# Kernel optimization log

Measured on AMD Instinct MI355X. Metric: run time of the kernel, lower is better.

## Reference

```python
import jax, jax.numpy as jnp
import numpy as np

N_HEADS = 32
N_KV_HEADS = 8
HEAD_DIM = 128
HIDDEN = 4096
ROPE_BASE = 10000.0


def _rope_tables(seq_len, head_dim, base):
    inv_freq = 1.0 / (base ** (jnp.arange(0, head_dim, 2, dtype=jnp.float32) / head_dim))
    t = jnp.arange(seq_len, dtype=jnp.float32)
    freqs = jnp.outer(t, inv_freq)                    # (S, D/2)
    emb = jnp.concatenate([freqs, freqs], axis=-1)    # (S, D)
    return jnp.cos(emb), jnp.sin(emb)


def _rotate_half(x):
    half = x.shape[-1] // 2
    return jnp.concatenate([-x[..., half:], x[..., :half]], axis=-1)


def _apply_rope(x, cos, sin):
    # x: (B, H, S, D); cos/sin: (S, D)
    return x * cos[None, None] + _rotate_half(x) * sin[None, None]


def setup_inputs() -> dict:
    key = jax.random.key(0)
    k1, k2, k3 = jax.random.split(key, 3)
    bsz, q_len = 2, 2048
    total_heads = N_HEADS + 2 * N_KV_HEADS
    hidden_states = jax.random.normal(k1, (bsz, q_len, HIDDEN), dtype=jnp.float32)
    w_qkv = jax.random.normal(k2, (total_heads * HEAD_DIM, HIDDEN), dtype=jnp.float32) * 0.02
    w_o = jax.random.normal(k3, (HIDDEN, N_HEADS * HEAD_DIM), dtype=jnp.float32) * 0.02
    return {"hidden_states": hidden_states, "w_qkv": w_qkv, "w_o": w_o}


def reference(hidden_states, w_qkv, w_o):
    bsz, q_len, _ = hidden_states.shape
    n_rep = N_HEADS // N_KV_HEADS

    qkv = jnp.einsum('bsh,oh->bso', hidden_states, w_qkv)  # (B, S, total_heads*D)
    q_sz = N_HEADS * HEAD_DIM
    kv_sz = N_KV_HEADS * HEAD_DIM
    q = qkv[..., :q_sz].reshape(bsz, q_len, N_HEADS, HEAD_DIM).transpose(0, 2, 1, 3)
    k = qkv[..., q_sz:q_sz + kv_sz].reshape(bsz, q_len, N_KV_HEADS, HEAD_DIM).transpose(0, 2, 1, 3)
    v = qkv[..., q_sz + kv_sz:].reshape(bsz, q_len, N_KV_HEADS, HEAD_DIM).transpose(0, 2, 1, 3)

    cos, sin = _rope_tables(q_len, HEAD_DIM, ROPE_BASE)
    q = _apply_rope(q, cos, sin)
    k = _apply_rope(k, cos, sin)

    # repeat KV heads for GQA
    k = jnp.repeat(k, n_rep, axis=1)  # (B, H, S, D)
    v = jnp.repeat(v, n_rep, axis=1)

    scale = HEAD_DIM ** -0.5
    scores = jnp.einsum('bhqd,bhkd->bhqk', q, k) * scale
    causal = jnp.tril(jnp.ones((q_len, q_len), dtype=bool))
    scores = jnp.where(causal[None, None], scores, jnp.finfo(scores.dtype).min)
    attn = jax.nn.softmax(scores, axis=-1)
    out = jnp.einsum('bhqk,bhkd->bhqd', attn, v)  # (B, H, S, D)
    out = out.transpose(0, 2, 1, 3).reshape(bsz, q_len, N_HEADS * HEAD_DIM)
    return jnp.einsum('bso,ho->bsh', out, w_o)
```

## Files before the change

kernel.cpp:

```cpp
#include <hip/hip_runtime.h>
#include <stdint.h>

#define N_HEADS   32
#define N_KV      8
#define HEAD_DIM  128
#define HIDDEN_DIM 4096
#define BSZ       2
#define SEQ       2048
#define TOT_HEADS 48
#define QKV_DIM   6144
#define ROWS      4096
#define ROPE_HEADS 40

typedef __attribute__((ext_vector_type(4)))  float f32x4;
typedef __attribute__((ext_vector_type(16))) float f32x16;
typedef __attribute__((ext_vector_type(8)))  short bf16x8;
typedef unsigned short u16;
typedef unsigned int   u32;

#define AS1 __attribute__((address_space(1)))
#define AS3 __attribute__((address_space(3)))

static __device__ __forceinline__ float bf16f(u16 u) { return __uint_as_float(((u32)u) << 16); }
static __device__ __forceinline__ u16 f2bf(float f) {
  u32 x = __float_as_uint(f);
  x += 0x7fffu + ((x >> 16) & 1u);
  return (u16)(x >> 16);
}
static __device__ __forceinline__ u32 cvt_pk_bf16(float lo, float hi) {
  u32 r;
  asm("v_cvt_pk_bf16_f32 %0, %1, %2" : "=v"(r) : "v"(lo), "v"(hi));
  return r;
}
static __device__ __forceinline__ bf16x8 mk8(u32 a, u32 b, u32 c, u32 d) {
  union { u32 u[4]; bf16x8 v; } x;
  x.u[0] = a; x.u[1] = b; x.u[2] = c; x.u[3] = d;
  return x.v;
}
static __device__ __forceinline__ void pl32swap(u32& a, u32& b) {
  asm("v_permlane32_swap_b32 %0, %1" : "+v"(a), "+v"(b));
}
static __device__ __forceinline__ float crosshalf_max(float v) {
  u32 xa = __float_as_uint(v), xb;
  asm("v_mov_b32 %0, %1" : "=v"(xb) : "v"(xa));
  pl32swap(xa, xb);
  return fmaxf(__uint_as_float(xa), __uint_as_float(xb));
}
static __device__ __forceinline__ float crosshalf_sum(float v) {
  u32 xa = __float_as_uint(v), xb;
  asm("v_mov_b32 %0, %1" : "=v"(xb) : "v"(xa));
  pl32swap(xa, xb);
  return __uint_as_float(xa) + __uint_as_float(xb);
}

#define SBAR()  do { __builtin_amdgcn_sched_barrier(0); __builtin_amdgcn_s_barrier(); \
                     __builtin_amdgcn_sched_barrier(0); } while (0)
#define LGKM0() do { asm volatile("s_waitcnt lgkmcnt(0)" ::: "memory"); \
                     __builtin_amdgcn_sched_barrier(0); } while (0)

__global__ void cast3_k(const float4* __restrict__ a, const float4* __restrict__ b,
                        const float4* __restrict__ c,
                        ushort4* __restrict__ oa, ushort4* __restrict__ ob,
                        ushort4* __restrict__ oc, int na, int nb, int nc) {
  int i = blockIdx.x * blockDim.x + threadIdx.x;
  const int stride = gridDim.x * blockDim.x;
  const int tot = na + nb + nc;
  for (; i < tot; i += stride) {
    const float4* s; ushort4* d; int j = i;
    if (j < na)           { s = a; d = oa; }
    else if (j < na + nb) { s = b; d = ob; j -= na; }
    else                  { s = c; d = oc; j -= na + nb; }
    const float4 v = s[j];
    ushort4 o;
    o.x = f2bf(v.x); o.y = f2bf(v.y); o.z = f2bf(v.z); o.w = f2bf(v.w);
    d[j] = o;
  }
}

__global__ void rope_tables_k(float* __restrict__ ctab, float* __restrict__ stab) {
  int t = blockIdx.x * blockDim.x + threadIdx.x;
  if (t >= SEQ * 64) return;
  int s = t >> 6, i = t & 63;
  float inv = powf(10000.0f, -(float)i / 64.0f);
  float ang = (float)s * inv;
  float sv, cv;
  sincosf(ang, &sv, &cv);
  ctab[t] = cv; stab[t] = sv;
}

template<int F32OUT>
__global__ __launch_bounds__(256, 2)
void gemm_bt_k(const u16* __restrict__ A, const u16* __restrict__ Bw,
               void* __restrict__ C, int M, int N, int K, int ldc)
{
  __shared__ uint4 smA[1024];
  __shared__ uint4 smB[1024];
  const int tid = threadIdx.x;
  const int nbx = N >> 7;
  const int bm = (blockIdx.x / nbx) << 7;
  const int bn = (blockIdx.x % nbx) << 7;
  const int lane = tid & 63;
  const int wave = tid >> 6;
  const int wm = (wave >> 1) << 6;
  const int wn = (wave & 1) << 6;
  const int fr = lane & 15;
  const int fq = lane >> 4;

  f32x4 acc[4][4];
#pragma unroll
  for (int i = 0; i < 4; ++i)
#pragma unroll
    for (int j = 0; j < 4; ++j)
      acc[i][j] = {0.f, 0.f, 0.f, 0.f};

  const int gl_r = lane >> 3;
  const int gl_c = (lane & 7) ^ gl_r;

  for (int k0 = 0; k0 < K; k0 += 64) {
#pragma unroll
    for (int i = 0; i < 4; ++i) {
      const int rbase = (wave << 5) + (i << 3);
      const int row = rbase + gl_r;
      const u16* gA = A  + (size_t)(bm + row) * K + k0 + (gl_c << 3);
      const u16* gB = Bw + (size_t)(bn + row) * K + k0 + (gl_c << 3);
      __builtin_amdgcn_global_load_lds((const AS1 u32*)gA, (AS3 u32*)&smA[rbase << 3], 16, 0, 0);
      __builtin_amdgcn_global_load_lds((const AS1 u32*)gB, (AS3 u32*)&smB[rbase << 3], 16, 0, 0);
    }
    __syncthreads();
#pragma unroll
    for (int kk = 0; kk < 2; ++kk) {
      bf16x8 af[4], bfr[4];
      const int cc = (kk << 2) + fq;
#pragma unroll
      for (int m = 0; m < 4; ++m) {
        const int row = wm + (m << 4) + fr;
        af[m] = *reinterpret_cast<const bf16x8*>(&smA[(row << 3) + (cc ^ (row & 7))]);
      }
#pragma unroll
      for (int n = 0; n < 4; ++n) {
        const int row = wn + (n << 4) + fr;
        bfr[n] = *reinterpret_cast<const bf16x8*>(&smB[(row << 3) + (cc ^ (row & 7))]);
      }
#pragma unroll
      for (int m = 0; m < 4; ++m)
#pragma unroll
        for (int n = 0; n < 4; ++n)
          acc[m][n] = __builtin_amdgcn_mfma_f32_16x16x32_bf16(af[m], bfr[n], acc[m][n], 0, 0, 0);
    }
    __syncthreads();
  }

  const int col0 = bn + wn + fr;
#pragma unroll
  for (int m = 0; m < 4; ++m) {
#pragma unroll
    for (int i = 0; i < 4; ++i) {
      const int row = bm + wm + (m << 4) + (fq << 2) + i;
      if (F32OUT) {
        float* rp = reinterpret_cast<float*>(C) + (size_t)row * ldc + col0;
#pragma unroll
        for (int n = 0; n < 4; ++n) rp[n << 4] = acc[m][n][i];
      } else {
        u16* rp = reinterpret_cast<u16*>(C) + (size_t)row * ldc + col0;
#pragma unroll
        for (int n = 0; n < 4; ++n) rp[n << 4] = f2bf(acc[m][n][i]);
      }
    }
  }
}

template<int F32OUT>
__global__ __launch_bounds__(512, 2)
void gemm256_k(const u16* __restrict__ A, const u16* __restrict__ Bw,
               void* __restrict__ C, int M, int N, int K, int ldc)
{
  extern __shared__ uint4 lds[];
  uint4* LA = lds;
  uint4* LB = lds + 4096;
  const int NT = K >> 6;
  const int tid  = threadIdx.x;
  const int lane = tid & 63;
  const int wave = tid >> 6;
  const int nbx = N >> 8;
  const int cpx = gridDim.x >> 3;
  const int wg  = (blockIdx.x & 7) * cpx + (blockIdx.x >> 3);
  const int bm = (wg / nbx) << 8;
  const int bn = (wg % nbx) << 8;

  const int wm = (wave >> 2) << 7;
  const int wn = (wave & 3) << 6;
  const int fr = lane & 15;
  const int fq = lane >> 4;
  const int s7 = fr & 7;

  const int rA  = (wave << 3) + (lane >> 3);
  const int c8e = (((lane & 7) ^ (lane >> 3)) << 3);

  auto SA = [&](int t, int h, int buf) {
    uint4* d = LA + (buf << 11) + (h << 10) + (wave << 6);
    const u16* s = A + (size_t)(bm + (h << 7) + rA) * K + (t << 6) + c8e;
    __builtin_amdgcn_global_load_lds((const AS1 u32*)s, (AS3 u32*)d, 16, 0, 0);
    __builtin_amdgcn_global_load_lds((const AS1 u32*)(s + (size_t)64 * K), (AS3 u32*)(d + 512), 16, 0, 0);
  };
  auto SB = [&](int t, int h, int buf) {
    uint4* d = LB + (buf << 11) + (h << 10) + (wave << 6);
    const u16* s = Bw + (size_t)(bn + (h << 7) + rA) * K + (t << 6) + c8e;
    __builtin_amdgcn_global_load_lds((const AS1 u32*)s, (AS3 u32*)d, 16, 0, 0);
    __builtin_amdgcn_global_load_lds((const AS1 u32*)(s + (size_t)64 * K), (AS3 u32*)(d + 512), 16, 0, 0);
  };

  f32x4 acc[8][4];
#pragma unroll
  for (int m = 0; m < 8; ++m)
#pragma unroll
    for (int n = 0; n < 4; ++n)
      acc[m][n] = {0.f, 0.f, 0.f, 0.f};

  SB(0, 0, 0); SB(0, 1, 0); SA(0, 0, 0); SA(0, 1, 0);
  SB(1, 0, 1); SB(1, 1, 1); SA(1, 0, 1);
  asm volatile("s_waitcnt vmcnt(6)" ::: "memory");
  SBAR();

  bf16x8 Af[4][2], B0[2][2], B1[2][2];

#pragma unroll 1
  for (int t = 0; t < NT; ++t) {
    const int buf  = t & 1;
    const int base = buf << 11;
    const int abase = base + ((wm + fr) << 3);
    const int bbase = base + ((wn + fr) << 3);

#pragma unroll
    for (int m = 0; m < 4; ++m)
#pragma unroll
      for (int kk = 0; kk < 2; ++kk)
        Af[m][kk] = *reinterpret_cast<const bf16x8*>(&LA[abase + m * 128 + (((kk << 2) + fq) ^ s7)]);
#pragma unroll
    for (int n = 0; n < 2; ++n)
#pragma unroll
      for (int kk = 0; kk < 2; ++kk)
        B0[n][kk] = *reinterpret_cast<const bf16x8*>(&LB[bbase + n * 128 + (((kk << 2) + fq) ^ s7)]);
    if (t + 1 < NT) SA(t + 1, 1, buf ^ 1);
    SBAR();
    LGKM0();
    __builtin_amdgcn_s_setprio(1);
#pragma unroll
    for (int m = 0; m < 4; ++m)
#pragma unroll
      for (int n = 0; n < 2; ++n)
#pragma unroll
        for (int kk = 0; kk < 2; ++kk)
          acc[m][n] = __builtin_amdgcn_mfma_f32_16x16x32_bf16(Af[m][kk], B0[n][kk], acc[m][n], 0, 0, 0);
    __builtin_amdgcn_s_setprio(0);
    SBAR();

#pragma unroll
    for (int n = 0; n < 2; ++n)
#pragma unroll
      for (int kk = 0; kk < 2; ++kk)
        B1[n][kk] = *reinterpret_cast<const bf16x8*>(&LB[bbase + (2 + n) * 128 + (((kk << 2) + fq) ^ s7)]);
    SBAR();
    LGKM0();
    __builtin_amdgcn_s_setprio(1);
#pragma unroll
    for (int m = 0; m < 4; ++m)
#pragma unroll
      for (int n = 0; n < 2; ++n)
#pragma unroll
        for (int kk = 0; kk < 2; ++kk)
          acc[m][2 + n] = __builtin_amdgcn_mfma_f32_16x16x32_bf16(Af[m][kk], B1[n][kk], acc[m][2 + n], 0, 0, 0);
    __builtin_amdgcn_s_setprio(0);
    SBAR();

#pragma unroll
    for (int m = 0; m < 4; ++m)
#pragma unroll
      for (int kk = 0; kk < 2; ++kk)
        Af[m][kk] = *reinterpret_cast<const bf16x8*>(&LA[abase + 512 + m * 128 + (((kk << 2) + fq) ^ s7)]);
    if (t + 2 < NT) SB(t + 2, 0, buf);
    SBAR();
    LGKM0();
    __builtin_amdgcn_s_setprio(1);
#pragma unroll
    for (int m = 0; m < 4; ++m)
#pragma unroll
      for (int n = 0; n < 2; ++n)
#pragma unroll
        for (int kk = 0; kk < 2; ++kk)
          acc[4 + m][2 + n] = __builtin_amdgcn_mfma_f32_16x16x32_bf16(Af[m][kk], B1[n][kk], acc[4 + m][2 + n], 0, 0, 0);
    __builtin_amdgcn_s_setprio(0);
    SBAR();

    if (t + 2 < NT) { SB(t + 2, 1, buf); SA(t + 2, 0, buf); }
    __builtin_amdgcn_s_setprio(1);
#pragma unroll
    for (int m = 0; m < 4; ++m)
#pragma unroll
      for (int n = 0; n < 2; ++n)
#pragma unroll
        for (int kk = 0; kk < 2; ++kk)
          acc[4 + m][n] = __builtin_amdgcn_mfma_f32_16x16x32_bf16(Af[m][kk], B0[n][kk], acc[4 + m][n], 0, 0, 0);
    __builtin_amdgcn_s_setprio(0);
    if (t < NT - 2)       { asm volatile("s_waitcnt vmcnt(6)" ::: "memory"); }
    else if (t == NT - 2) { asm volatile("s_waitcnt vmcnt(0)" ::: "memory"); }
    SBAR();
  }

  const int col0 = bn + wn + fr;
#pragma unroll
  for (int m = 0; m < 8; ++m) {
#pragma unroll
    for (int i = 0; i < 4; ++i) {
      const int row = bm + wm + (m << 4) + (fq << 2) + i;
      if (F32OUT) {
        float* rp = reinterpret_cast<float*>(C) + (size_t)row * ldc + col0;
#pragma unroll
        for (int n = 0; n < 4; ++n) rp[n << 4] = acc[m][n][i];
      } else {
        u16* rp = reinterpret_cast<u16*>(C) + (size_t)row * ldc + col0;
#pragma unroll
        for (int n = 0; n < 4; ++n) rp[n << 4] = f2bf(acc[m][n][i]);
      }
    }
  }
}

__global__ void rope_scatter_k(const u16* __restrict__ QKV,
                               const float* __restrict__ ctab, const float* __restrict__ stab,
                               u16* __restrict__ Qo, u16* __restrict__ Ko)
{
  const int t = blockIdx.x * blockDim.x + threadIdx.x;
  const int d = t & 63;
  const int hh = (t >> 6) % ROPE_HEADS;
  const int row = t / (64 * ROPE_HEADS);
  const int b = row >> 11, sq = row & (SEQ - 1);
  const u16* src = QKV + (size_t)row * QKV_DIM + hh * HEAD_DIM;
  const float x1 = bf16f(src[d]);
  const float x2 = bf16f(src[d + 64]);
  const float c = ctab[(sq << 6) + d], sn = stab[(sq << 6) + d];
  float y1 = x1 * c - x2 * sn;
  float y2 = x2 * c + x1 * sn;
  u16* dst;
  if (hh < N_HEADS) {
    const float SC2 = 0.1275170747f;
    y1 *= SC2; y2 *= SC2;
    dst = Qo + ((size_t)(b * N_HEADS + hh) * SEQ + sq) * HEAD_DIM;
  } else {
    dst = Ko + ((size_t)(b * N_KV + (hh - N_HEADS)) * SEQ + sq) * HEAD_DIM;
  }
  dst[d] = f2bf(y1);
  dst[d + 64] = f2bf(y2);
}

__global__ __launch_bounds__(256)
void vtrans_k(const u16* __restrict__ QKV, u16* __restrict__ Vt)
{
  __shared__ u16 tile[64][72];
  const int idx = blockIdx.x;
  const int dt = idx & 1;
  const int st = (idx >> 1) & 31;
  const int kv = (idx >> 6) & 7;
  const int b  = idx >> 9;
  const int tid = threadIdx.x;
  const int s0 = st << 6, d0 = dt << 6;
  const int rl = tid >> 3, cc8 = (tid & 7) << 3;
#pragma unroll
  for (int p = 0; p < 2; ++p) {
    const int sl = rl + (p << 5);
    const u16* src = QKV + (size_t)(b * SEQ + s0 + sl) * QKV_DIM
                   + (N_HEADS + N_KV + kv) * HEAD_DIM + d0 + cc8;
    *reinterpret_cast<uint4*>(&tile[sl][cc8]) = *reinterpret_cast<const uint4*>(src);
  }
  __syncthreads();
#pragma unroll
  for (int p = 0; p < 2; ++p) {
    const int dl = rl + (p << 5);
    u16 tmp[8];
#pragma unroll
    for (int k2 = 0; k2 < 8; ++k2) tmp[k2] = tile[cc8 + k2][dl];
    u16* dst = Vt + ((size_t)(b * N_KV + kv) * HEAD_DIM + d0 + dl) * SEQ + s0 + cc8;
    *reinterpret_cast<uint4*>(dst) = *reinterpret_cast<const uint4*>(tmp);
  }
}

__global__ __launch_bounds__(512, 2)
void attn_mfma_k(const u16* __restrict__ Q, const u16* __restrict__ K,
                 const u16* __restrict__ Vt, u16* __restrict__ Out)
{
  __shared__ uint4 Ksm[2][1024];
  __shared__ uint4 Vsm[2][1024];
  const int tid  = threadIdx.x;
  const int lane = tid & 63;
  const int w    = tid >> 6;
  const int idx  = blockIdx.x;
  const int kvh  = idx & 7;
  const int b    = (idx >> 3) & 1;
  const int qi   = 31 - (idx >> 4);
  const int q0   = qi << 6;
  const int head = w & 3;
  const int qsub = w >> 2;
  const int h    = (kvh << 2) + head;

  const int ql = lane & 31;
  const int hh = lane >> 5;

  const u16* Qh = Q  + (size_t)(b * N_HEADS + h) * SEQ * HEAD_DIM;
  const u16* Kb = K  + (size_t)(b * N_KV + kvh) * SEQ * HEAD_DIM;
  const u16* Vb = Vt + (size_t)(b * N_KV + kvh) * HEAD_DIM * SEQ;

  int koff[8];
#pragma unroll
  for (int f = 0; f < 8; ++f) koff[f] = (ql << 4) + (((f << 1) + hh) ^ (ql & 15));
  int voff[4][4];
#pragma unroll
  for (int dblk = 0; dblk < 4; ++dblk)
#pragma unroll
    for (int j = 0; j < 4; ++j)
      voff[dblk][j] = ((((dblk << 5) + ql) << 3)) + (((j << 1) + hh + ql) & 7);

  auto stage = [&](int buf, int ks) {
#pragma unroll
    for (int p = 0; p < 2; ++p) {
      const int base = (p << 9) + (w << 6);
      const int sl2 = base + lane;
      const int row = sl2 >> 4, cs = sl2 & 15;
      const int g = cs ^ (row & 15);
      const u16* src = Kb + (size_t)(ks + row) * HEAD_DIM + (g << 3);
      __builtin_amdgcn_global_load_lds((const AS1 u32*)src, (AS3 u32*)&Ksm[buf][base], 16, 0, 0);
    }
#pragma unroll
    for (int p = 0; p < 2; ++p) {
      const int base = (p << 9) + (w << 6);
      const int sl2 = base + lane;
      const int d = sl2 >> 3, cs = sl2 & 7;
      const int g = (cs - d) & 7;
      const u16* src = Vb + (size_t)d * SEQ + ks + (g << 3);
      __builtin_amdgcn_global_load_lds((const AS1 u32*)src, (AS3 u32*)&Vsm[buf][base], 16, 0, 0);
    }
  };

  bf16x8 qf[8];
#pragma unroll
  for (int f = 0; f < 8; ++f)
    qf[f] = *reinterpret_cast<const bf16x8*>(Qh + (size_t)(q0 + (qsub << 5) + ql) * HEAD_DIM
                                             + 16 * f + 8 * hh);

  f32x16 o[4];
#pragma unroll
  for (int dblk = 0; dblk < 4; ++dblk)
#pragma unroll
    for (int r = 0; r < 16; ++r) o[dblk][r] = 0.f;
  float m2 = -1e30f, lsum = 0.f;

  stage(0, 0);

#pragma unroll 1
  for (int sb = 0; sb <= qi; ++sb) {
    const int cur = sb & 1;
    __syncthreads();
    if (sb < qi) stage(cur ^ 1, (sb + 1) << 6);

    f32x16 T0, T1;
#pragma unroll
    for (int r = 0; r < 16; ++r) { T0[r] = 0.f; T1[r] = 0.f; }
    __builtin_amdgcn_s_setprio(1);
#pragma unroll
    for (int f = 0; f < 8; ++f) {
      const bf16x8 kf = *reinterpret_cast<const bf16x8*>(&Ksm[cur][koff[f]]);
      T0 = __builtin_amdgcn_mfma_f32_32x32x16_bf16(kf, qf[f], T0, 0, 0, 0);
    }
#pragma unroll
    for (int f = 0; f < 8; ++f) {
      const bf16x8 kf = *reinterpret_cast<const bf16x8*>(&Ksm[cur][koff[f] + 512]);
      T1 = __builtin_amdgcn_mfma_f32_32x32x16_bf16(kf, qf[f], T1, 0, 0, 0);
    }
    __builtin_amdgcn_s_setprio(0);

    if (sb == qi) {
      const int limit = (qsub << 5) + ql;
#pragma unroll
      for (int r = 0; r < 16; ++r) {
        const int kr = (r & 3) + ((r >> 2) << 3) + (hh << 2);
        if (kr > limit)      T0[r] = -1e30f;
        if (kr + 32 > limit) T1[r] = -1e30f;
      }
    }
    float mx[8];
#pragma unroll
    for (int r = 0; r < 8; ++r)
      mx[r] = fmaxf(fmaxf(T0[2 * r], T0[2 * r + 1]), fmaxf(T1[2 * r], T1[2 * r + 1]));
#pragma unroll
    for (int r = 0; r < 4; ++r) mx[r] = fmaxf(mx[r], mx[r + 4]);
    mx[0] = fmaxf(mx[0], mx[2]);
    mx[1] = fmaxf(mx[1], mx[3]);
    const float mt = crosshalf_max(fmaxf(mx[0], mx[1]));

    if (__any(mt > m2 + 8.f)) {
      const float mnew = fmaxf(m2, mt);
      const float resc = exp2f(m2 - mnew);
      lsum *= resc;
#pragma unroll
      for (int r = 0; r < 16; ++r) {
        const int qr = (r & 3) + ((r >> 2) << 3) + (hh << 2);
        const float rr = __shfl(resc, qr);
#pragma unroll
        for (int dblk = 0; dblk < 4; ++dblk) o[dblk][r] *= rr;
      }
      m2 = mnew;
    }

    float ps = 0.f;
#pragma unroll
    for (int r = 0; r < 16; ++r) {
      const float p0 = exp2f(T0[r] - m2); T0[r] = p0; ps += p0;
      const float p1 = exp2f(T1[r] - m2); T1[r] = p1; ps += p1;
    }
    lsum += crosshalf_sum(ps);

    u32 pk[16];
#pragma unroll
    for (int i = 0; i < 8; ++i) {
      pk[i]     = cvt_pk_bf16(T0[2 * i], T0[2 * i + 1]);
      pk[8 + i] = cvt_pk_bf16(T1[2 * i], T1[2 * i + 1]);
    }
    pl32swap(pk[0], pk[2]);  pl32swap(pk[1], pk[3]);
    pl32swap(pk[4], pk[6]);  pl32swap(pk[5], pk[7]);
    pl32swap(pk[8], pk[10]); pl32swap(pk[9], pk[11]);
    pl32swap(pk[12], pk[14]); pl32swap(pk[13], pk[15]);
    bf16x8 a[4];
    a[0] = mk8(pk[0], pk[1], pk[2], pk[3]);
    a[1] = mk8(pk[4], pk[5], pk[6], pk[7]);
    a[2] = mk8(pk[8], pk[9], pk[10], pk[11]);
    a[3] = mk8(pk[12], pk[13], pk[14], pk[15]);

    __builtin_amdgcn_s_setprio(1);
#pragma unroll
    for (int dblk = 0; dblk < 4; ++dblk)
#pragma unroll
      for (int j = 0; j < 4; ++j) {
        const bf16x8 vb = *reinterpret_cast<const bf16x8*>(&Vsm[cur][voff[dblk][j]]);
        o[dblk] = __builtin_amdgcn_mfma_f32_32x32x16_bf16(a[j], vb, o[dblk], 0, 0, 0);
      }
    __builtin_amdgcn_s_setprio(0);
  }

  u16* Ob = Out + (size_t)(b * SEQ + q0 + (qsub << 5)) * HIDDEN_DIM + h * HEAD_DIM + ql;
#pragma unroll
  for (int r = 0; r < 16; ++r) {
    const int qr = (r & 3) + ((r >> 2) << 3) + (hh << 2);
    const float il = 1.0f / __shfl(lsum, qr);
    u16* rp = Ob + (size_t)qr * HIDDEN_DIM;
#pragma unroll
    for (int dblk = 0; dblk < 4; ++dblk)
      rp[dblk * 32] = f2bf(o[dblk][r] * il);
  }
}

extern "C" void kernel_launch(void* const* d_in, const int* in_sizes, int n_in,
                              void* d_out, int out_size, void* d_ws, size_t ws_size,
                              hipStream_t stream)
{
  const float* hs   = (const float*)d_in[0];
  const float* wqkv = (const float*)d_in[1];
  const float* wo   = (const float*)d_in[2];
  float* out = (float*)d_out;
  char* ws = (char*)d_ws;
  size_t off = 0;
  auto alloc = [&](size_t bytes) -> void* {
    void* p = ws + off;
    off += (bytes + 255) & ~(size_t)255;
    return p;
  };
  u16* Xbf    = (u16*)alloc((size_t)ROWS * HIDDEN_DIM * 2);
  u16* Wqkvbf = (u16*)alloc((size_t)QKV_DIM * HIDDEN_DIM * 2);
  u16* Wobf   = (u16*)alloc((size_t)HIDDEN_DIM * HIDDEN_DIM * 2);
  u16* QKVbf  = (u16*)alloc((size_t)ROWS * QKV_DIM * 2);
  u16* Qbf    = (u16*)alloc((size_t)BSZ * N_HEADS * SEQ * HEAD_DIM * 2);
  u16* Kbf    = (u16*)alloc((size_t)BSZ * N_KV * SEQ * HEAD_DIM * 2);
  u16* Vtbf   = (u16*)alloc((size_t)BSZ * N_KV * SEQ * HEAD_DIM * 2);
  float* ctab = (float*)alloc((size_t)SEQ * 64 * 4);
  float* stab = (float*)alloc((size_t)SEQ * 64 * 4);
  u16* AOut   = (u16*)alloc((size_t)ROWS * HIDDEN_DIM * 2);
  if (off > ws_size) return;

  (void)hipFuncSetAttribute(reinterpret_cast<const void*>(&gemm256_k<0>),
                            hipFuncAttributeMaxDynamicSharedMemorySize, 131072);
  (void)hipFuncSetAttribute(reinterpret_cast<const void*>(&gemm256_k<1>),
                            hipFuncAttributeMaxDynamicSharedMemorySize, 131072);

  cast3_k<<<4096, 256, 0, stream>>>((const float4*)hs, (const float4*)wqkv, (const float4*)wo,
                                    (ushort4*)Xbf, (ushort4*)Wqkvbf, (ushort4*)Wobf,
                                    ROWS * HIDDEN_DIM / 4, QKV_DIM * HIDDEN_DIM / 4,
                                    HIDDEN_DIM * HIDDEN_DIM / 4);
  rope_tables_k<<<(SEQ * 64) / 256, 256, 0, stream>>>(ctab, stab);

  gemm256_k<0><<<(ROWS / 256) * (4096 / 256), 512, 131072, stream>>>(
      Xbf, Wqkvbf, (void*)QKVbf, ROWS, 4096, HIDDEN_DIM, QKV_DIM);
  gemm_bt_k<0><<<(ROWS / 128) * (2048 / 128), 256, 0, stream>>>(
      Xbf, Wqkvbf + (size_t)4096 * HIDDEN_DIM, (void*)(QKVbf + 4096),
      ROWS, 2048, HIDDEN_DIM, QKV_DIM);

  rope_scatter_k<<<ROWS * ROPE_HEADS * 64 / 256, 256, 0, stream>>>(QKVbf, ctab, stab, Qbf, Kbf);
  vtrans_k<<<BSZ * N_KV * (SEQ / 64) * (HEAD_DIM / 64), 256, 0, stream>>>(QKVbf, Vtbf);
  attn_mfma_k<<<BSZ * N_KV * (SEQ / 64), 512, 0, stream>>>(Qbf, Kbf, Vtbf, AOut);
  gemm256_k<1><<<(ROWS / 256) * (HIDDEN_DIM / 256), 512, 131072, stream>>>(
      AOut, Wobf, (void*)out, ROWS, HIDDEN_DIM, HIDDEN_DIM, HIDDEN_DIM);
}
```

Baseline: 508.6 us.

## Restructure GEMM main loop from four MFMA phases into two with full B fragments

The inner loop of the bf16 GEMM kernel now loads all four B fragments at once and runs two compute phases, one per half of A, instead of four quarter phases. This removes two block barriers and LDS wait points per K-step and issues all next-stage global-to-LDS loads in a single group. In exchange it holds more B fragment registers, which may lower occupancy. It also changes the vmcnt wait thresholds, which must still guarantee that buffers are filled before they are read.

```diff
diff --git a/kernel.cpp b/kernel.cpp
--- a/kernel.cpp
+++ b/kernel.cpp
@@ -221,7 +221,7 @@
   asm volatile("s_waitcnt vmcnt(6)" ::: "memory");
   SBAR();
 
-  bf16x8 Af[4][2], B0[2][2], B1[2][2];
+  bf16x8 Af[4][2], Bf[4][2];
 
 #pragma unroll 1
   for (int t = 0; t < NT; ++t) {
@@ -236,10 +236,10 @@
       for (int kk = 0; kk < 2; ++kk)
         Af[m][kk] = *reinterpret_cast<const bf16x8*>(&LA[abase + m * 128 + (((kk << 2) + fq) ^ s7)]);
 #pragma unroll
-    for (int n = 0; n < 2; ++n)
+    for (int n = 0; n < 4; ++n)
 #pragma unroll
       for (int kk = 0; kk < 2; ++kk)
-        B0[n][kk] = *reinterpret_cast<const bf16x8*>(&LB[bbase + n * 128 + (((kk << 2) + fq) ^ s7)]);
+        Bf[n][kk] = *reinterpret_cast<const bf16x8*>(&LB[bbase + n * 128 + (((kk << 2) + fq) ^ s7)]);
     if (t + 1 < NT) SA(t + 1, 1, buf ^ 1);
     SBAR();
     LGKM0();
@@ -247,61 +247,32 @@
 #pragma unroll
     for (int m = 0; m < 4; ++m)
 #pragma unroll
-      for (int n = 0; n < 2; ++n)
+      for (int n = 0; n < 4; ++n)
 #pragma unroll
         for (int kk = 0; kk < 2; ++kk)
-          acc[m][n] = __builtin_amdgcn_mfma_f32_16x16x32_bf16(Af[m][kk], B0[n][kk], acc[m][n], 0, 0, 0);
+          acc[m][n] = __builtin_amdgcn_mfma_f32_16x16x32_bf16(Af[m][kk], Bf[n][kk], acc[m][n], 0, 0, 0);
     __builtin_amdgcn_s_setprio(0);
+    asm volatile("s_waitcnt vmcnt(8)" ::: "memory");
     SBAR();
 
 #pragma unroll
-    for (int n = 0; n < 2; ++n)
+    for (int m = 0; m < 4; ++m)
 #pragma unroll
       for (int kk = 0; kk < 2; ++kk)
-        B1[n][kk] = *reinterpret_cast<const bf16x8*>(&LB[bbase + (2 + n) * 128 + (((kk << 2) + fq) ^ s7)]);
+        Af[m][kk] = *reinterpret_cast<const bf16x8*>(&LA[abase + 512 + m * 128 + (((kk << 2) + fq) ^ s7)]);
+    if (t + 2 < NT) { SB(t + 2, 0, buf); SB(t + 2, 1, buf); SA(t + 2, 0, buf); }
     SBAR();
     LGKM0();
     __builtin_amdgcn_s_setprio(1);
 #pragma unroll
     for (int m = 0; m < 4; ++m)
 #pragma unroll
-      for (int n = 0; n < 2; ++n)
+      for (int n = 0; n < 4; ++n)
 #pragma unroll
         for (int kk = 0; kk < 2; ++kk)
-          acc[m][2 + n] = __builtin_amdgcn_mfma_f32_16x16x32_bf16(Af[m][kk], B1[n][kk], acc[m][2 + n], 0, 0, 0);
+          acc[4 + m][n] = __builtin_amdgcn_mfma_f32_16x16x32_bf16(Af[m][kk], Bf[n][kk], acc[4 + m][n], 0, 0, 0);
     __builtin_amdgcn_s_setprio(0);
-    SBAR();
-
-#pragma unroll
-    for (int m = 0; m < 4; ++m)
-#pragma unroll
-      for (int kk = 0; kk < 2; ++kk)
-        Af[m][kk] = *reinterpret_cast<const bf16x8*>(&LA[abase + 512 + m * 128 + (((kk << 2) + fq) ^ s7)]);
-    if (t + 2 < NT) SB(t + 2, 0, buf);
-    SBAR();
-    LGKM0();
-    __builtin_amdgcn_s_setprio(1);
-#pragma unroll
-    for (int m = 0; m < 4; ++m)
-#pragma unroll
-      for (int n = 0; n < 2; ++n)
-#pragma unroll
-        for (int kk = 0; kk < 2; ++kk)
-          acc[4 + m][2 + n] = __builtin_amdgcn_mfma_f32_16x16x32_bf16(Af[m][kk], B1[n][kk], acc[4 + m][2 + n], 0, 0, 0);
-    __builtin_amdgcn_s_setprio(0);
-    SBAR();
-
-    if (t + 2 < NT) { SB(t + 2, 1, buf); SA(t + 2, 0, buf); }
-    __builtin_amdgcn_s_setprio(1);
-#pragma unroll
-    for (int m = 0; m < 4; ++m)
-#pragma unroll
-      for (int n = 0; n < 2; ++n)
-#pragma unroll
-        for (int kk = 0; kk < 2; ++kk)
-          acc[4 + m][n] = __builtin_amdgcn_mfma_f32_16x16x32_bf16(Af[m][kk], B0[n][kk], acc[4 + m][n], 0, 0, 0);
-    __builtin_amdgcn_s_setprio(0);
-    if (t < NT - 2)       { asm volatile("s_waitcnt vmcnt(6)" ::: "memory"); }
+    if (t < NT - 2)       { asm volatile("s_waitcnt vmcnt(8)" ::: "memory"); }
     else if (t == NT - 2) { asm volatile("s_waitcnt vmcnt(0)" ::: "memory"); }
     SBAR();
   }
```

After: 516.3 us. No clear change (+1.5%).
